# Kernel optimization log

Hardware: AMD Instinct MI355X
Metric: run time of the kernel (lower is better)

The kernel has to match this reference:

```python
import jax, jax.numpy as jnp
import numpy as np

# LLaMA-7B style BitNet b1.58 MLP dims
B, S = 2, 2048
H, I = 4096, 11008
EPS = 1e-8
QMAX = 127.0  # int8 activation range


def _ternary_weight(key, shape):
    """BitNet b1.58 absmean weight quantization: per-tensor scale, ternary {-1,0,1}."""
    w = jax.random.normal(key, shape, jnp.float32) * 0.02
    ws = jnp.mean(jnp.abs(w)) + EPS
    qw = jnp.clip(jnp.round(w / ws), -1.0, 1.0)
    return qw, ws


def setup_inputs() -> dict:
    key = jax.random.key(0)
    k0, k1, k2, k3 = jax.random.split(key, 4)
    # x arrives already absmean-quantized to int8 values (stored as float) + scalar scale
    xf = jax.random.normal(k0, (B, S, H), jnp.float32)
    xs = jnp.mean(jnp.abs(xf)) + EPS
    x = jnp.clip(jnp.round(xf / xs), -QMAX - 1, QMAX)
    qw_gate, ws_gate = _ternary_weight(k1, (I, H))
    qw_up, ws_up = _ternary_weight(k2, (I, H))
    qw_down, ws_down = _ternary_weight(k3, (H, I))
    return {"x": x, "x_scale": xs,
            "qw_gate": qw_gate, "ws_gate": ws_gate,
            "qw_up": qw_up, "ws_up": ws_up,
            "qw_down": qw_down, "ws_down": ws_down}


def absmean_quantize(x):
    """Per-tensor absmean quantization to int8 range with straight-through rounding."""
    scale = jnp.mean(jnp.abs(x)) + EPS
    c = x / scale
    q = c + jax.lax.stop_gradient(jnp.clip(jnp.round(c), -QMAX - 1, QMAX) - c)
    return q, scale


def quantized_linear(xq, xs, qw, ws):
    # integer-valued GEMM; output scale is product of input and weight scales
    out = jnp.einsum('bsh,ih->bsi', xq, qw)
    return out, xs * ws


def reference(x, x_scale, qw_gate, ws_gate, qw_up, ws_up, qw_down, ws_down):
    gate, gate_s = quantized_linear(x, x_scale, qw_gate, ws_gate)      # [B,S,I]
    up, up_s = quantized_linear(x, x_scale, qw_up, ws_up)              # [B,S,I]
    # quantized_act: dequant -> SiLU -> re-quantize (absmean)
    ga_q, ga_s = absmean_quantize(jax.nn.silu(gate * gate_s))
    # quantized elementwise matmul: multiply q-values, multiply scales, re-quantize
    inter_q, inter_s = absmean_quantize(ga_q * up * (ga_s * up_s))
    # down projection (I -> H): einsum over intermediate dim
    out = jnp.einsum('bsi,hi->bsh', inter_q, qw_down)
    return out, inter_s * ws_down
```

## Files before the change

### kernel.cpp

```cpp
#include <hip/hip_runtime.h>
#include <math.h>

#define TOK 4096
#define HD  4096
#define ID  11008

typedef int i32x4 __attribute__((ext_vector_type(4)));
typedef float f32x4v __attribute__((ext_vector_type(4)));
typedef char i8x4v __attribute__((ext_vector_type(4)));

#define GLDS16(g, l) __builtin_amdgcn_global_load_lds( \
    (const __attribute__((address_space(1))) void*)(g), \
    (__attribute__((address_space(3))) void*)(l), 16, 0, 0)

__global__ void conv_all(const float* __restrict__ x,  char* __restrict__ xq,
                         const float* __restrict__ wg, char* __restrict__ wgq,
                         const float* __restrict__ wu, char* __restrict__ wuq,
                         const float* __restrict__ wd, char* __restrict__ wdq)
{
  const long NX = (long)TOK * HD / 4, NW = (long)ID * HD / 4;
  const long total = NX + 3 * NW;
  const long stride = (long)gridDim.x * blockDim.x;
  for (long i = (long)blockIdx.x * blockDim.x + threadIdx.x; i < total;
       i += stride) {
    const f32x4v* src; i8x4v* dst; long j;
    if (i < NX)               { src = (const f32x4v*)x;  dst = (i8x4v*)xq;  j = i; }
    else if (i < NX + NW)     { src = (const f32x4v*)wg; dst = (i8x4v*)wgq; j = i - NX; }
    else if (i < NX + 2 * NW) { src = (const f32x4v*)wu; dst = (i8x4v*)wuq; j = i - NX - NW; }
    else                      { src = (const f32x4v*)wd; dst = (i8x4v*)wdq; j = i - NX - 2 * NW; }
    f32x4v v = __builtin_nontemporal_load(&src[j]);
    i8x4v o;
    o.x = (char)(int)rintf(v.x);
    o.y = (char)(int)rintf(v.y);
    o.z = (char)(int)rintf(v.z);
    o.w = (char)(int)rintf(v.w);
    dst[j] = o;
  }
}

template<int MODE>
__global__ __launch_bounds__(256, 3)
void gemm_i8(const char* __restrict__ A,
             const char* __restrict__ Bm,
             int M, int N, int K,
             float* __restrict__ Cout,
             const float* __restrict__ ga_in,
             const float* __restrict__ sc0,
             const float* __restrict__ sc1,
             double* __restrict__ sums,
             long long NN)
{
  __shared__ char As[16384];
  __shared__ char Bs[16384];
  __shared__ double red[4];

  const int tid  = threadIdx.x;
  const int w    = tid >> 6;
  const int lane = tid & 63;
  const int wr   = lane & 15;
  const int qd   = lane >> 4;
  const int wm   = (w >> 1) << 6;
  const int wn   = (w & 1) << 6;

  const int L   = blockIdx.y * gridDim.x + blockIdx.x;
  const int xcd = L & 7;
  const int r   = L >> 3;
  const int m0  = (xcd + ((r & 3) << 3)) << 7;
  const int n0  = (r >> 2) << 7;

  i32x4 acc[4][4] = {};

  const int rowL = tid >> 3;
  const int chk  = (tid & 7) ^ (rowL & 7);
  const char* gA = A  + (size_t)(m0 + rowL) * K + (chk << 4);
  const char* gB = Bm + (size_t)(n0 + rowL) * K + (chk << 4);
  const size_t rk32 = (size_t)32 * K;
  char* lA = As + (w << 10);
  char* lB = Bs + (w << 10);

  const int s7    = wr & 7;
  const int abase = ((wm + wr) << 7) + ((qd ^ s7) << 4);
  const int bbase = ((wn + wr) << 7) + ((qd ^ s7) << 4);

  for (int k0 = 0; k0 < K; k0 += 128) {
    GLDS16(gA + k0,            lA);
    GLDS16(gA + k0 +     rk32, lA + 4096);
    GLDS16(gA + k0 + 2 * rk32, lA + 8192);
    GLDS16(gA + k0 + 3 * rk32, lA + 12288);
    GLDS16(gB + k0,            lB);
    GLDS16(gB + k0 +     rk32, lB + 4096);
    GLDS16(gB + k0 + 2 * rk32, lB + 8192);
    GLDS16(gB + k0 + 3 * rk32, lB + 12288);
    __syncthreads();

#pragma unroll
    for (int h = 0; h < 2; h++) {
      const int hx = h << 6;
      i32x4 af[4], bfr[4];
#pragma unroll
      for (int i = 0; i < 4; i++)
        af[i] = *(const i32x4*)(As + ((abase + (i << 11)) ^ hx));
#pragma unroll
      for (int j = 0; j < 4; j++)
        bfr[j] = *(const i32x4*)(Bs + ((bbase + (j << 11)) ^ hx));

#pragma unroll
      for (int i = 0; i < 4; i++)
#pragma unroll
        for (int j = 0; j < 4; j++)
          acc[i][j] = __builtin_amdgcn_mfma_i32_16x16x64_i8(af[i], bfr[j],
                                                            acc[i][j], 0, 0, 0);
    }
    __syncthreads();
  }

  double lsum = 0.0;

  if (MODE == 0) {
    const float gs = sc0[0] * sc1[0];
#pragma unroll
    for (int i = 0; i < 4; i++) {
      const int mb = m0 + wm + (i << 4) + (qd << 2);
#pragma unroll
      for (int j = 0; j < 4; j++) {
        const int n = n0 + wn + (j << 4) + wr;
#pragma unroll
        for (int r2 = 0; r2 < 4; r2++) {
          float g = (float)acc[i][j][r2] * gs;
          float s = g / (1.0f + expf(-g));
          __builtin_nontemporal_store(s, &Cout[(size_t)(mb + r2) * N + n]);
          lsum += (double)fabsf(s);
        }
      }
    }
  } else if (MODE == 1) {
    const float up_s  = sc0[0] * sc1[0];
    const float ga_s  = (float)(sums[0] / (double)NN) + 1e-8f;
    const float combo = ga_s * up_s;
#pragma unroll
    for (int i = 0; i < 4; i++) {
      const int mb = m0 + wm + (i << 4) + (qd << 2);
#pragma unroll
      for (int j = 0; j < 4; j++) {
        const int n = n0 + wn + (j << 4) + wr;
#pragma unroll
        for (int r2 = 0; r2 < 4; r2++) {
          float up = (float)acc[i][j][r2];
          float ga = __builtin_nontemporal_load(
                         &ga_in[(size_t)(mb + r2) * N + n]);
          float gq = fmaxf(-128.0f, fminf(127.0f, rintf(ga / ga_s)));
          float itv = gq * up * combo;
          __builtin_nontemporal_store(itv, &Cout[(size_t)(mb + r2) * N + n]);
          lsum += (double)fabsf(itv);
        }
      }
    }
  } else {
#pragma unroll
    for (int i = 0; i < 4; i++) {
      const int mb = m0 + wm + (i << 4) + (qd << 2);
#pragma unroll
      for (int j = 0; j < 4; j++) {
        const int n = n0 + wn + (j << 4) + wr;
#pragma unroll
        for (int r2 = 0; r2 < 4; r2++)
          __builtin_nontemporal_store((float)acc[i][j][r2],
                                      &Cout[(size_t)(mb + r2) * N + n]);
      }
    }
  }

  if (MODE != 2) {
    for (int off = 32; off; off >>= 1) lsum += __shfl_down(lsum, off, 64);
    if (lane == 0) red[w] = lsum;
    __syncthreads();
    if (tid == 0) atomicAdd(&sums[MODE], red[0] + red[1] + red[2] + red[3]);
  }
}

__global__ void quant_inter(const float* __restrict__ inter,
                            char* __restrict__ outq,
                            const double* __restrict__ sums, long long NN,
                            const float* __restrict__ wsd,
                            float* __restrict__ scalar_out, int n4)
{
  const float is = (float)(sums[1] / (double)NN) + 1e-8f;
  if (blockIdx.x == 0 && threadIdx.x == 0) scalar_out[0] = is * wsd[0];
  int stride = gridDim.x * blockDim.x;
  for (int i = blockIdx.x * blockDim.x + threadIdx.x; i < n4; i += stride) {
    f32x4v v = __builtin_nontemporal_load(&((const f32x4v*)inter)[i]);
    i8x4v o;
    o.x = (char)(int)fmaxf(-128.0f, fminf(127.0f, rintf(v.x / is)));
    o.y = (char)(int)fmaxf(-128.0f, fminf(127.0f, rintf(v.y / is)));
    o.z = (char)(int)fmaxf(-128.0f, fminf(127.0f, rintf(v.z / is)));
    o.w = (char)(int)fmaxf(-128.0f, fminf(127.0f, rintf(v.w / is)));
    ((i8x4v*)outq)[i] = o;
  }
}

extern "C" void kernel_launch(void* const* d_in, const int* in_sizes, int n_in,
                              void* d_out, int out_size, void* d_ws, size_t ws_size,
                              hipStream_t stream) {
  const float* x        = (const float*)d_in[0];
  const float* x_scale  = (const float*)d_in[1];
  const float* qw_gate  = (const float*)d_in[2];
  const float* ws_gate  = (const float*)d_in[3];
  const float* qw_up    = (const float*)d_in[4];
  const float* ws_up    = (const float*)d_in[5];
  const float* qw_down  = (const float*)d_in[6];
  const float* ws_down  = (const float*)d_in[7];
  float* out = (float*)d_out;

  char* ws = (char*)d_ws;
  double* sums = (double*)ws;
  size_t off = 256;
  char* xq     = ws + off; off += (size_t)TOK * HD;
  char* wgq    = ws + off; off += (size_t)ID * HD;
  char* wuq    = ws + off; off += (size_t)ID * HD;
  char* wdq    = ws + off; off += (size_t)HD * ID;
  char* interq = ws + off; off += (size_t)TOK * ID;
  float* ga    = (float*)(ws + off); off += (size_t)TOK * ID * 4;
  float* inter = (float*)(ws + off); off += (size_t)TOK * ID * 4;

  const long long NN = (long long)TOK * ID;

  (void)hipMemsetAsync(sums, 0, 16, stream);

  conv_all<<<8192, 256, 0, stream>>>(x, xq, qw_gate, wgq, qw_up, wuq,
                                     qw_down, wdq);

  gemm_i8<0><<<dim3(ID / 128, TOK / 128), 256, 0, stream>>>(
      xq, wgq, TOK, ID, HD, ga, nullptr, x_scale, ws_gate, sums, NN);

  gemm_i8<1><<<dim3(ID / 128, TOK / 128), 256, 0, stream>>>(
      xq, wuq, TOK, ID, HD, inter, ga, x_scale, ws_up, sums, NN);

  quant_inter<<<8192, 256, 0, stream>>>(inter, interq, sums, NN, ws_down,
                                        out + (size_t)TOK * HD, (int)(NN / 4));

  gemm_i8<2><<<dim3(HD / 128, TOK / 128), 256, 0, stream>>>(
      interq, wdq, TOK, HD, ID, out, nullptr, nullptr, nullptr, sums, NN);
}
```

Baseline: 1.124 ms.

## Double-buffer A tile in LDS and stream B fragments directly into registers

The GEMM now keeps two 16KB LDS buffers for the A tile and prefetches the next K-slice with global_load_lds while the current one is consumed, which removes one barrier per iteration. The B operand no longer goes through LDS: each lane loads its MFMA fragments straight from global memory into registers, one half-step ahead. This is meant to overlap global latency with MFMA work and cut LDS traffic. In exchange it raises register pressure and makes B loads uncoalesced and redundant across the waves that share the same columns.

```diff
diff --git a/kernel.cpp b/kernel.cpp
--- a/kernel.cpp
+++ b/kernel.cpp
@@ -50,8 +50,7 @@
              double* __restrict__ sums,
              long long NN)
 {
-  __shared__ char As[16384];
-  __shared__ char Bs[16384];
+  __shared__ char As[32768];
   __shared__ double red[4];
 
   const int tid  = threadIdx.x;
@@ -72,46 +71,80 @@
 
   const int rowL = tid >> 3;
   const int chk  = (tid & 7) ^ (rowL & 7);
-  const char* gA = A  + (size_t)(m0 + rowL) * K + (chk << 4);
-  const char* gB = Bm + (size_t)(n0 + rowL) * K + (chk << 4);
+  const char* gA = A + (size_t)(m0 + rowL) * K + (chk << 4);
   const size_t rk32 = (size_t)32 * K;
-  char* lA = As + (w << 10);
-  char* lB = Bs + (w << 10);
+  const int ldst = w << 10;
 
   const int s7    = wr & 7;
   const int abase = ((wm + wr) << 7) + ((qd ^ s7) << 4);
-  const int bbase = ((wn + wr) << 7) + ((qd ^ s7) << 4);
-
-  for (int k0 = 0; k0 < K; k0 += 128) {
-    GLDS16(gA + k0,            lA);
-    GLDS16(gA + k0 +     rk32, lA + 4096);
-    GLDS16(gA + k0 + 2 * rk32, lA + 8192);
-    GLDS16(gA + k0 + 3 * rk32, lA + 12288);
-    GLDS16(gB + k0,            lB);
-    GLDS16(gB + k0 +     rk32, lB + 4096);
-    GLDS16(gB + k0 + 2 * rk32, lB + 8192);
-    GLDS16(gB + k0 + 3 * rk32, lB + 12288);
+
+  const char* pB = Bm + (size_t)(n0 + wn + wr) * K + (qd << 4);
+  const size_t bj = (size_t)16 * K;
+
+  i32x4 Bp[2][4];
+
+  {
+    char* lA = As + ldst;
+    GLDS16(gA,            lA);
+    GLDS16(gA +     rk32, lA + 4096);
+    GLDS16(gA + 2 * rk32, lA + 8192);
+    GLDS16(gA + 3 * rk32, lA + 12288);
+  }
+#pragma unroll
+  for (int j = 0; j < 4; j++)
+    Bp[0][j] = *(const i32x4*)(pB + j * bj);
+
+  const int nst = K >> 7;
+  int p = 0;
+  for (int s = 0; s < nst; s++) {
+    const int k0 = s << 7;
     __syncthreads();
-
-#pragma unroll
-    for (int h = 0; h < 2; h++) {
-      const int hx = h << 6;
-      i32x4 af[4], bfr[4];
-#pragma unroll
-      for (int i = 0; i < 4; i++)
-        af[i] = *(const i32x4*)(As + ((abase + (i << 11)) ^ hx));
+    if (s + 1 < nst) {
+      char* lA = As + ((p ^ 1) << 14) + ldst;
+      const char* g = gA + k0 + 128;
+      GLDS16(g,            lA);
+      GLDS16(g +     rk32, lA + 4096);
+      GLDS16(g + 2 * rk32, lA + 8192);
+      GLDS16(g + 3 * rk32, lA + 12288);
+    }
+    const char* base = As + (p << 14);
+
+#pragma unroll
+    for (int j = 0; j < 4; j++)
+      Bp[1][j] = *(const i32x4*)(pB + k0 + 64 + j * bj);
+
+    {
+      i32x4 af[4];
+#pragma unroll
+      for (int i = 0; i < 4; i++)
+        af[i] = *(const i32x4*)(base + abase + (i << 11));
+#pragma unroll
+      for (int i = 0; i < 4; i++)
+#pragma unroll
+        for (int j = 0; j < 4; j++)
+          acc[i][j] = __builtin_amdgcn_mfma_i32_16x16x64_i8(af[i], Bp[0][j],
+                                                            acc[i][j], 0, 0, 0);
+    }
+
+    if (s + 1 < nst) {
 #pragma unroll
       for (int j = 0; j < 4; j++)
-        bfr[j] = *(const i32x4*)(Bs + ((bbase + (j << 11)) ^ hx));
-
+        Bp[0][j] = *(const i32x4*)(pB + k0 + 128 + j * bj);
+    }
+
+    {
+      i32x4 af[4];
+#pragma unroll
+      for (int i = 0; i < 4; i++)
+        af[i] = *(const i32x4*)(base + ((abase + (i << 11)) ^ 64));
 #pragma unroll
       for (int i = 0; i < 4; i++)
 #pragma unroll
         for (int j = 0; j < 4; j++)
-          acc[i][j] = __builtin_amdgcn_mfma_i32_16x16x64_i8(af[i], bfr[j],
+          acc[i][j] = __builtin_amdgcn_mfma_i32_16x16x64_i8(af[i], Bp[1][j],
                                                             acc[i][j], 0, 0, 0);
     }
-    __syncthreads();
+    p ^= 1;
   }
 
   double lsum = 0.0;
```

Result: slower. 1.722 ms (+53.2%).

## Double-buffer LDS tiles in int8 GEMM and drop nontemporal epilogue stores

Applied to the files above, without the earlier changes.

Doubles the shared-memory A/B tiles so the next K-slice is prefetched with global_load_lds while MFMAs consume the current buffer, and removes the trailing barrier per iteration. Occupancy is lowered from 3 to 2 blocks per CU to fit the larger LDS footprint. Epilogue loads and stores switch from nontemporal to regular accesses, which may help the ga buffer stay in cache between the gate and up GEMMs. The risk is reduced occupancy, and the single barrier must still order the async LDS writes correctly.

```diff
diff --git a/kernel.cpp b/kernel.cpp
--- a/kernel.cpp
+++ b/kernel.cpp
@@ -39,7 +39,7 @@
 }
 
 template<int MODE>
-__global__ __launch_bounds__(256, 3)
+__global__ __launch_bounds__(256, 2)
 void gemm_i8(const char* __restrict__ A,
              const char* __restrict__ Bm,
              int M, int N, int K,
@@ -50,8 +50,8 @@
              double* __restrict__ sums,
              long long NN)
 {
-  __shared__ char As[16384];
-  __shared__ char Bs[16384];
+  __shared__ char As[32768];
+  __shared__ char Bs[32768];
   __shared__ double red[4];
 
   const int tid  = threadIdx.x;
@@ -75,23 +75,46 @@
   const char* gA = A  + (size_t)(m0 + rowL) * K + (chk << 4);
   const char* gB = Bm + (size_t)(n0 + rowL) * K + (chk << 4);
   const size_t rk32 = (size_t)32 * K;
-  char* lA = As + (w << 10);
-  char* lB = Bs + (w << 10);
+  const int ldst = w << 10;
 
   const int s7    = wr & 7;
   const int abase = ((wm + wr) << 7) + ((qd ^ s7) << 4);
   const int bbase = ((wn + wr) << 7) + ((qd ^ s7) << 4);
 
-  for (int k0 = 0; k0 < K; k0 += 128) {
-    GLDS16(gA + k0,            lA);
-    GLDS16(gA + k0 +     rk32, lA + 4096);
-    GLDS16(gA + k0 + 2 * rk32, lA + 8192);
-    GLDS16(gA + k0 + 3 * rk32, lA + 12288);
-    GLDS16(gB + k0,            lB);
-    GLDS16(gB + k0 +     rk32, lB + 4096);
-    GLDS16(gB + k0 + 2 * rk32, lB + 8192);
-    GLDS16(gB + k0 + 3 * rk32, lB + 12288);
+  {
+    char* lA = As + ldst;
+    char* lB = Bs + ldst;
+    GLDS16(gA,            lA);
+    GLDS16(gA +     rk32, lA + 4096);
+    GLDS16(gA + 2 * rk32, lA + 8192);
+    GLDS16(gA + 3 * rk32, lA + 12288);
+    GLDS16(gB,            lB);
+    GLDS16(gB +     rk32, lB + 4096);
+    GLDS16(gB + 2 * rk32, lB + 8192);
+    GLDS16(gB + 3 * rk32, lB + 12288);
+  }
+
+  const int nst = K >> 7;
+  int p = 0;
+  for (int s = 0; s < nst; s++) {
     __syncthreads();
+
+    if (s + 1 < nst) {
+      const int k1 = (s + 1) << 7;
+      char* lA = As + ((p ^ 1) << 14) + ldst;
+      char* lB = Bs + ((p ^ 1) << 14) + ldst;
+      GLDS16(gA + k1,            lA);
+      GLDS16(gA + k1 +     rk32, lA + 4096);
+      GLDS16(gA + k1 + 2 * rk32, lA + 8192);
+      GLDS16(gA + k1 + 3 * rk32, lA + 12288);
+      GLDS16(gB + k1,            lB);
+      GLDS16(gB + k1 +     rk32, lB + 4096);
+      GLDS16(gB + k1 + 2 * rk32, lB + 8192);
+      GLDS16(gB + k1 + 3 * rk32, lB + 12288);
+    }
+
+    const char* baseA = As + (p << 14);
+    const char* baseB = Bs + (p << 14);
 
 #pragma unroll
     for (int h = 0; h < 2; h++) {
@@ -99,10 +122,10 @@
       i32x4 af[4], bfr[4];
 #pragma unroll
       for (int i = 0; i < 4; i++)
-        af[i] = *(const i32x4*)(As + ((abase + (i << 11)) ^ hx));
+        af[i] = *(const i32x4*)(baseA + ((abase + (i << 11)) ^ hx));
 #pragma unroll
       for (int j = 0; j < 4; j++)
-        bfr[j] = *(const i32x4*)(Bs + ((bbase + (j << 11)) ^ hx));
+        bfr[j] = *(const i32x4*)(baseB + ((bbase + (j << 11)) ^ hx));
 
 #pragma unroll
       for (int i = 0; i < 4; i++)
@@ -111,7 +134,7 @@
           acc[i][j] = __builtin_amdgcn_mfma_i32_16x16x64_i8(af[i], bfr[j],
                                                             acc[i][j], 0, 0, 0);
     }
-    __syncthreads();
+    p ^= 1;
   }
 
   double lsum = 0.0;
@@ -128,7 +151,7 @@
         for (int r2 = 0; r2 < 4; r2++) {
           float g = (float)acc[i][j][r2] * gs;
           float s = g / (1.0f + expf(-g));
-          __builtin_nontemporal_store(s, &Cout[(size_t)(mb + r2) * N + n]);
+          Cout[(size_t)(mb + r2) * N + n] = s;
           lsum += (double)fabsf(s);
         }
       }
@@ -146,11 +169,10 @@
 #pragma unroll
         for (int r2 = 0; r2 < 4; r2++) {
           float up = (float)acc[i][j][r2];
-          float ga = __builtin_nontemporal_load(
-                         &ga_in[(size_t)(mb + r2) * N + n]);
+          float ga = ga_in[(size_t)(mb + r2) * N + n];
           float gq = fmaxf(-128.0f, fminf(127.0f, rintf(ga / ga_s)));
           float itv = gq * up * combo;
-          __builtin_nontemporal_store(itv, &Cout[(size_t)(mb + r2) * N + n]);
+          Cout[(size_t)(mb + r2) * N + n] = itv;
           lsum += (double)fabsf(itv);
         }
       }
@@ -164,8 +186,7 @@
         const int n = n0 + wn + (j << 4) + wr;
 #pragma unroll
         for (int r2 = 0; r2 < 4; r2++)
-          __builtin_nontemporal_store((float)acc[i][j][r2],
-                                      &Cout[(size_t)(mb + r2) * N + n]);
+          Cout[(size_t)(mb + r2) * N + n] = (float)acc[i][j][r2];
       }
     }
   }
```

Measured after the change: 1.377 ms. 1.22x slower.
